# Kernel tuning notes

Measured on AMD Instinct MI355X. Metric: run time of the kernel, lower is better.

The kernel has to match this reference:

```python
import jax, jax.numpy as jnp
import numpy as np

N_NODES = 100000
N_EDGES = 1000000
IN_F, HID_F, OUT_F = 128, 128, 16


def setup_inputs() -> dict:
    key = jax.random.key(0)
    ks = jax.random.split(key, 8)
    x = jax.random.normal(ks[0], (N_NODES, IN_F), dtype=jnp.float32)
    src = jax.random.randint(ks[1], (N_EDGES,), 0, N_NODES, dtype=jnp.int64)
    dst = jax.random.randint(ks[2], (N_EDGES,), 0, N_NODES, dtype=jnp.int64)
    s = 1.0 / np.sqrt(HID_F)
    W1 = jax.random.normal(ks[3], (IN_F, HID_F), dtype=jnp.float32) * s
    W2 = jax.random.normal(ks[4], (HID_F, HID_F), dtype=jnp.float32) * s
    W3 = jax.random.normal(ks[5], (HID_F, HID_F), dtype=jnp.float32) * s
    W4 = jax.random.normal(ks[6], (HID_F, HID_F), dtype=jnp.float32) * s
    W5 = jax.random.normal(ks[7], (HID_F, OUT_F), dtype=jnp.float32) * s
    return {
        "x": x, "src": src, "dst": dst,
        "W1": W1, "b1": jnp.zeros((HID_F,), jnp.float32),
        "W2": W2, "b2": jnp.zeros((HID_F,), jnp.float32),
        "W3": W3, "b3": jnp.zeros((HID_F,), jnp.float32),
        "W4": W4, "b4": jnp.zeros((HID_F,), jnp.float32),
        "W5": W5, "b5": jnp.zeros((OUT_F,), jnp.float32),
    }


def reference(x, src, dst, W1, b1, W2, b2, W3, b3, W4, b4, W5, b5):
    N = x.shape[0]
    # in-degree per destination node (static graph, computed once)
    deg = jax.ops.segment_sum(jnp.ones_like(dst, dtype=x.dtype), dst, num_segments=N)
    inv = (1.0 / (deg + 1.0))[:, None]  # gcn aggregator normalizer: 1/(deg_in+1)

    def sage_gcn(h, W, b):
        # h_neigh[v] = (h[v] + sum_{u->v} h[u]) / (deg_in(v)+1); then linear
        agg = (h + jax.ops.segment_sum(h[src], dst, num_segments=N)) * inv
        return agg @ W + b

    h = jax.nn.relu(sage_gcn(x, W1, b1))
    h = jax.nn.relu(sage_gcn(h, W2, b2))
    h = jax.nn.relu(sage_gcn(h, W3, b3))
    h = jax.nn.relu(sage_gcn(h, W4, b4))
    h = sage_gcn(h, W5, b5)
    return jax.nn.log_softmax(h, axis=-1)
```

## Files before the change

### kernel.cpp

```cpp
#include <hip/hip_runtime.h>
#include <hip/hip_bf16.h>

#define NNODES 100000
#define NP (NNODES + 8)
#define NEDGES 1000000
#define HID 128
#define OUTF 16
#define NB 16
#define BCAP 81920
#define KB 64
#define BZT 1024
#define DB2 32
#define NBINS (NB * DB2)
#define NSL 4

typedef __attribute__((ext_vector_type(8))) short short8;
typedef __attribute__((ext_vector_type(4))) float floatx4;
typedef __attribute__((ext_vector_type(4))) unsigned int uintx4;
typedef unsigned int uint32;
typedef unsigned long long ull;
typedef unsigned short ushort16;

__device__ __forceinline__ float blo(uint32 u) { return __uint_as_float(u << 16); }
__device__ __forceinline__ float bhi(uint32 u) { return __uint_as_float(u & 0xffff0000u); }
__device__ __forceinline__ ushort16 f2b(float f) {
    __hip_bfloat16 h = __float2bfloat16(f);
    return *reinterpret_cast<ushort16*>(&h);
}
__device__ __forceinline__ uint32 pack2(float a, float b) {
    return (uint32)f2b(a) | ((uint32)f2b(b) << 16);
}


__global__ __launch_bounds__(BZT) void bucketize(const int* __restrict__ src,
                                                 const int* __restrict__ dst,
                                                 int* __restrict__ bcursor,
                                                 ull* __restrict__ stage, int E) {
    __shared__ int cnt[NB], lbase[NB], gbase[NB];
    __shared__ int2 buf[BZT];
    __shared__ unsigned char bb[BZT];
    int t = threadIdx.x;
    int e0 = blockIdx.x * BZT;
    int e = e0 + t;
    if (t < NB) cnt[t] = 0;
    __syncthreads();
    int s = 0, d = 0, b = 0, r = 0;
    bool valid = e < E;
    if (valid) {
        s = src[e];
        d = dst[e];
        b = (int)((unsigned)d * NB / NNODES);
        r = atomicAdd(&cnt[b], 1);
    }
    __syncthreads();
    if (t == 0) {
        int run = 0;
        for (int i = 0; i < NB; i++) { lbase[i] = run; run += cnt[i]; }
    }
    __syncthreads();
    if (valid) {
        int p = lbase[b] + r;
        buf[p] = make_int2(s, d);
        bb[p] = (unsigned char)b;
    }
    if (t < NB) gbase[t] = atomicAdd(&bcursor[t], cnt[t]);
    __syncthreads();
    int nvalid = min(BZT, E - e0);
    if (t < nvalid) {
        int b2 = bb[t];
        int2 sd = buf[t];
        int pos = gbase[b2] + (t - lbase[b2]);
        if (pos < BCAP) {
            ull val = (ull)(unsigned)sd.x | ((ull)(unsigned)sd.y << 32);
            __builtin_nontemporal_store(val, &stage[(size_t)b2 * BCAP + pos]);
        }
    }
}


__global__ __launch_bounds__(256) void count_rank(const ull* __restrict__ stage,
                                                  const int* __restrict__ bcursor,
                                                  int* __restrict__ counts,
                                                  int* __restrict__ rnk) {
    int blk = blockIdx.x;
    int b = (blk & 7) + 8 * ((blk >> 3) & 1);
    int slot = blk >> 4;
    int cntb = min(bcursor[b], BCAP);
    int per = (cntb + KB - 1) / KB;
    int s0 = slot * per;
    int s1 = min(s0 + per, cntb);
    const ull* st = stage + (size_t)b * BCAP;
    int* rk = rnk + (size_t)b * BCAP;
    for (int i = s0 + threadIdx.x; i < s1; i += 256) {
        ull v = st[i];
        int d = (int)(unsigned)(v >> 32);
        rk[i] = atomicAdd(&counts[d], 1);
    }
}


__global__ __launch_bounds__(256) void fill2(const ull* __restrict__ stage,
                                             const int* __restrict__ rnk,
                                             const int* __restrict__ bcursor,
                                             const int* __restrict__ perm,
                                             const int* __restrict__ offs,
                                             int* __restrict__ csr) {
    int blk = blockIdx.x;
    int b = (blk & 7) + 8 * ((blk >> 3) & 1);
    int slot = blk >> 4;
    int cntb = min(bcursor[b], BCAP);
    int per = (cntb + KB - 1) / KB;
    int s0 = slot * per;
    int s1 = min(s0 + per, cntb);
    const ull* st = stage + (size_t)b * BCAP;
    const int* rk = rnk + (size_t)b * BCAP;
    for (int i = s0 + threadIdx.x; i < s1; i += 256) {
        ull v = st[i];
        int s = (int)(v & 0xffffffffu);
        int d = (int)(unsigned)(v >> 32);
        int pd = perm[d];
        csr[offs[pd] + rk[i]] = perm[s];
    }
}


__global__ __launch_bounds__(256) void binhist(const int* __restrict__ counts,
                                               int* __restrict__ bins, int N) {
    __shared__ int h[NBINS];
    int t = threadIdx.x;
    for (int k = t; k < NBINS; k += 256) h[k] = 0;
    __syncthreads();
    int i = blockIdx.x * 256 + t;
    if (i < N) {
        int bi = (int)((unsigned)i * NB / NNODES);
        int db = min((counts[i] + 7) >> 3, DB2 - 1);
        atomicAdd(&h[bi * DB2 + db], 1);
    }
    __syncthreads();
    for (int k = t; k < NBINS; k += 256)
        if (h[k] > 0) atomicAdd(&bins[k], h[k]);
}

__global__ void binscan(int* __restrict__ bins) {
    if (threadIdx.x == 0) {
        int run = 0;
        for (int i = 0; i < NBINS; i++) {
            int c = bins[i];
            bins[i] = run;
            run += c;
        }
    }
}

__global__ __launch_bounds__(256) void dsort2(const int* __restrict__ counts,
                                              int* __restrict__ bins,
                                              int* __restrict__ perm,
                                              int* __restrict__ iperm,
                                              int* __restrict__ cnts_s, int N) {
    __shared__ int h[NBINS], lb[NBINS];
    int t = threadIdx.x;
    for (int k = t; k < NBINS; k += 256) h[k] = 0;
    __syncthreads();
    int i = blockIdx.x * 256 + t;
    int c = 0, idx = 0, r = 0;
    bool valid = i < N;
    if (valid) {
        c = counts[i];
        int bi = (int)((unsigned)i * NB / NNODES);
        idx = bi * DB2 + min((c + 7) >> 3, DB2 - 1);
        r = atomicAdd(&h[idx], 1);
    }
    __syncthreads();
    for (int k = t; k < NBINS; k += 256)
        lb[k] = (h[k] > 0) ? atomicAdd(&bins[k], h[k]) : 0;
    __syncthreads();
    if (valid) {
        int p = lb[idx] + r;
        perm[i] = p;
        iperm[p] = i;
        cnts_s[p] = c;
    }
}

__global__ void scan1(const int* __restrict__ cnts_s, int* __restrict__ offs,
                      int* __restrict__ bsum, int N) {
    __shared__ int tmp[256];
    int t = threadIdx.x;
    int i = blockIdx.x * 256 + t;
    int v = (i < N) ? ((cnts_s[i] + 7) & ~7) : 0;
    tmp[t] = v;
    __syncthreads();
    for (int d = 1; d < 256; d <<= 1) {
        int add = (t >= d) ? tmp[t - d] : 0;
        __syncthreads();
        tmp[t] += add;
        __syncthreads();
    }
    if (i < N) offs[i] = tmp[t] - v;
    if (t == 255) bsum[blockIdx.x] = tmp[255];
}

__global__ void scan2(int* __restrict__ bsum, int nb) {
    __shared__ int tmp[512];
    int t = threadIdx.x;
    int v = (t < nb) ? bsum[t] : 0;
    tmp[t] = v;
    __syncthreads();
    for (int d = 1; d < 512; d <<= 1) {
        int add = (t >= d) ? tmp[t - d] : 0;
        __syncthreads();
        tmp[t] += add;
        __syncthreads();
    }
    if (t < nb) bsum[t] = tmp[t] - v;
}

__global__ void scan3(int* __restrict__ offs, const int* __restrict__ bsum,
                      const int* __restrict__ cnts_s, float* __restrict__ invs,
                      int* __restrict__ csr, int N) {
    int i = blockIdx.x * 256 + threadIdx.x;
    if (i < N) {
        int o = offs[i] + bsum[blockIdx.x];
        offs[i] = o;
        int c = cnts_s[i];
        invs[i] = 1.0f / (float)(c + 1);
        int c8 = (c + 7) & ~7;
        for (int k = c; k < c8; k++) csr[o + k] = NNODES;
    }
}


__global__ void pack_all(const float* __restrict__ W1, const float* __restrict__ W2,
                         const float* __restrict__ W3, const float* __restrict__ W4,
                         ushort16* __restrict__ Wp1, ushort16* __restrict__ Wp2,
                         ushort16* __restrict__ Wp3, ushort16* __restrict__ Wp4,
                         uint32* __restrict__ zb, uint32* __restrict__ hb,
                         uint32* __restrict__ z16b) {
    int blk = blockIdx.x;
    int lane = threadIdx.x;
    if (blk < 128) {
        int w = blk >> 5, b = blk & 31;
        const float* W = w == 0 ? W1 : w == 1 ? W2 : w == 2 ? W3 : W4;
        ushort16* Wp = w == 0 ? Wp1 : w == 1 ? Wp2 : w == 2 ? Wp3 : Wp4;
        int nt = b >> 2, ks = b & 3;
        int n = nt * 16 + (lane & 15);
        int kbase = ks * 32 + ((lane >> 4) << 3);
        ushort16 tmp[8];
#pragma unroll
        for (int i = 0; i < 8; i++) tmp[i] = f2b(W[(size_t)(kbase + i) * HID + n]);
        *(uint4*)&Wp[((size_t)b * 64 + lane) * 8] = *(uint4*)tmp;
    } else {
        for (int i = lane; i < 4 * 8 * 16; i += 64) {
            int s = i >> 7, rem = i & 127, r = rem >> 4, k = rem & 15;
            zb[((size_t)s * NP + NNODES + r) * 16 + k] = 0;
            hb[((size_t)s * NP + NNODES + r) * 16 + k] = 0;
        }
        for (int i = lane; i < 64; i += 64)
            z16b[(size_t)(NNODES + (i >> 3)) * 8 + (i & 7)] = 0;
    }
}


template <int AF32>
__global__ __launch_bounds__(256) void gemm_mfma(const void* __restrict__ Av,
                                                 const int* __restrict__ iperm,
                                                 const ushort16* __restrict__ Wp,
                                                 ushort16* __restrict__ Z, int M) {
    __shared__ __align__(16) ushort16 Wl[32 * 64 * 8];
    int t = threadIdx.x;
    const uint4* wp4 = (const uint4*)Wp;
    uint4* wl4 = (uint4*)Wl;
#pragma unroll
    for (int p = 0; p < 8; p++) wl4[t + p * 256] = wp4[t + p * 256];
    __syncthreads();

    int wv = t >> 6, lane = t & 63;
    int row = blockIdx.x * 64 + wv * 16 + (lane & 15);
    int rowc = min(row, M - 1);
    int kb = (lane >> 4) << 3;

    short8 a[4];
    if (AF32) {
        const float* A = (const float*)Av;
        int orig = iperm[rowc];
#pragma unroll
        for (int ks = 0; ks < 4; ks++) {
            const float* p = A + (size_t)orig * HID + ks * 32 + kb;
            floatx4 lo = *(const floatx4*)p;
            floatx4 hi = *(const floatx4*)(p + 4);
            union { short8 s; ushort16 u[8]; } cv;
            cv.u[0] = f2b(lo.x); cv.u[1] = f2b(lo.y); cv.u[2] = f2b(lo.z); cv.u[3] = f2b(lo.w);
            cv.u[4] = f2b(hi.x); cv.u[5] = f2b(hi.y); cv.u[6] = f2b(hi.z); cv.u[7] = f2b(hi.w);
            a[ks] = cv.s;
        }
    } else {
        const ushort16* A = (const ushort16*)Av;
#pragma unroll
        for (int ks = 0; ks < 4; ks++)
            a[ks] = *(const short8*)(A + ((size_t)ks * NP + rowc) * 32 + kb);
    }

    floatx4 acc[8];
#pragma unroll
    for (int nt = 0; nt < 8; nt++) acc[nt] = (floatx4){0.f, 0.f, 0.f, 0.f};

#pragma unroll
    for (int nt = 0; nt < 8; nt++) {
#pragma unroll
        for (int ks = 0; ks < 4; ks++) {
            short8 w = *(const short8*)&Wl[(size_t)(((nt << 2) | ks) * 64 + lane) * 8];
            acc[nt] = __builtin_amdgcn_mfma_f32_16x16x32_bf16(w, a[ks], acc[nt], 0, 0, 0);
        }
    }

    if (row < M) {
        int c4 = (lane >> 4) << 2;
#pragma unroll
        for (int nt = 0; nt < 8; nt++) {
            int col = nt * 16 + c4;
            int sl = col >> 5, off = col & 31;
            union { ushort16 u[4]; uint2 v; } pk;
            pk.u[0] = f2b(acc[nt][0]);
            pk.u[1] = f2b(acc[nt][1]);
            pk.u[2] = f2b(acc[nt][2]);
            pk.u[3] = f2b(acc[nt][3]);
            *(uint2*)&Z[((size_t)sl * NP + row) * 32 + off] = pk.v;
        }
    }
}


#define ACCN(acc0, acc1, acc2, acc3, g)                \
    {                                                  \
        acc0.x += blo((g).x); acc0.y += bhi((g).x);    \
        acc1.x += blo((g).y); acc1.y += bhi((g).y);    \
        acc2.x += blo((g).z); acc2.y += bhi((g).z);    \
        acc3.x += blo((g).w); acc3.y += bhi((g).w);    \
    }

__global__ __launch_bounds__(256) void agg_sliced(const uint32* __restrict__ Z,
                                                  const int* __restrict__ offs,
                                                  const int* __restrict__ cnts_s,
                                                  const int* __restrict__ csr,
                                                  const float* __restrict__ invs,
                                                  const float* __restrict__ bias,
                                                  uint32* __restrict__ H, int N) {
    int s = blockIdx.x & 3;
    int chunk = blockIdx.x >> 2;
    int t = threadIdx.x;
    int l = t & 3;
    int p = chunk * 64 + (t >> 2);
    bool act = p < N;
    int pc = act ? p : N - 1;
    const uint4* Zs = (const uint4*)(Z + (size_t)s * NP * 16);
    uint4* Hs = (uint4*)(H + (size_t)s * NP * 16);

    int beg = offs[pc];
    int cnt8 = (cnts_s[pc] + 7) & ~7;
    float sc = invs[pc];

    uint4 sv = Zs[(size_t)pc * 4 + l];
    float2 acc0 = make_float2(blo(sv.x), bhi(sv.x));
    float2 acc1 = make_float2(blo(sv.y), bhi(sv.y));
    float2 acc2 = make_float2(blo(sv.z), bhi(sv.z));
    float2 acc3 = make_float2(blo(sv.w), bhi(sv.w));

    for (int j = 0; j < cnt8; j += 8) {
        int4 ia = *(const int4*)&csr[beg + j];
        int4 ib = *(const int4*)&csr[beg + j + 4];
        uint4 g[8];
        g[0] = Zs[(size_t)ia.x * 4 + l];
        g[1] = Zs[(size_t)ia.y * 4 + l];
        g[2] = Zs[(size_t)ia.z * 4 + l];
        g[3] = Zs[(size_t)ia.w * 4 + l];
        g[4] = Zs[(size_t)ib.x * 4 + l];
        g[5] = Zs[(size_t)ib.y * 4 + l];
        g[6] = Zs[(size_t)ib.z * 4 + l];
        g[7] = Zs[(size_t)ib.w * 4 + l];
#pragma unroll
        for (int q = 0; q < 8; q++) ACCN(acc0, acc1, acc2, acc3, g[q]);
    }

    const float* bp = bias + s * 32 + l * 8;
    floatx4 b01 = *(const floatx4*)bp;
    floatx4 b23 = *(const floatx4*)(bp + 4);
    uintx4 o;
    o.x = pack2(fmaxf(acc0.x * sc + b01.x, 0.f), fmaxf(acc0.y * sc + b01.y, 0.f));
    o.y = pack2(fmaxf(acc1.x * sc + b01.z, 0.f), fmaxf(acc1.y * sc + b01.w, 0.f));
    o.z = pack2(fmaxf(acc2.x * sc + b23.x, 0.f), fmaxf(acc2.y * sc + b23.y, 0.f));
    o.w = pack2(fmaxf(acc3.x * sc + b23.z, 0.f), fmaxf(acc3.y * sc + b23.w, 0.f));
    if (act) __builtin_nontemporal_store(o, (uintx4*)&Hs[(size_t)p * 4 + l]);
}


__global__ __launch_bounds__(256) void gemm16(const uint32* __restrict__ A,
                                              const float* __restrict__ W5,
                                              uint32* __restrict__ Z16, int M) {
    __shared__ float Ws[HID * OUTF];
    int t = threadIdx.x;
    for (int i = t; i < HID * OUTF; i += 256) Ws[i] = W5[i];
    __syncthreads();
    int gid = blockIdx.x * 256 + t;
    int r = gid >> 3, cp = gid & 7;
    if (r >= M) return;
    float a0 = 0.f, a1 = 0.f;
#pragma unroll
    for (int s4 = 0; s4 < 4; s4++) {
        const uint32* ar = A + ((size_t)s4 * NP + r) * 16;
#pragma unroll
        for (int k = 0; k < 16; k++) {
            uint32 u = ar[k];
            float f0 = blo(u), f1 = bhi(u);
            a0 += f0 * Ws[(s4 * 32 + 2 * k) * OUTF + 2 * cp] +
                  f1 * Ws[(s4 * 32 + 2 * k + 1) * OUTF + 2 * cp];
            a1 += f0 * Ws[(s4 * 32 + 2 * k) * OUTF + 2 * cp + 1] +
                  f1 * Ws[(s4 * 32 + 2 * k + 1) * OUTF + 2 * cp + 1];
        }
    }
    Z16[(size_t)r * 8 + cp] = pack2(a0, a1);
}


__global__ __launch_bounds__(256) void agg16_lsm(const uint32* __restrict__ Z16,
                                                 const int* __restrict__ offs,
                                                 const int* __restrict__ cnts_s,
                                                 const int* __restrict__ csr,
                                                 const float* __restrict__ invs,
                                                 const int* __restrict__ iperm,
                                                 const float* __restrict__ b5,
                                                 float* __restrict__ out, int N) {
    int t = threadIdx.x;
    int l = t & 1;
    int p = blockIdx.x * 128 + (t >> 1);
    bool act = p < N;
    int pc = act ? p : N - 1;
    const uint4* Zs = (const uint4*)Z16;

    uint4 sv = Zs[(size_t)pc * 2 + l];
    float2 acc0 = make_float2(blo(sv.x), bhi(sv.x));
    float2 acc1 = make_float2(blo(sv.y), bhi(sv.y));
    float2 acc2 = make_float2(blo(sv.z), bhi(sv.z));
    float2 acc3 = make_float2(blo(sv.w), bhi(sv.w));

    int beg = offs[pc];
    int cnt8 = (cnts_s[pc] + 7) & ~7;
    for (int j = 0; j < cnt8; j += 8) {
        int4 ia = *(const int4*)&csr[beg + j];
        int4 ib = *(const int4*)&csr[beg + j + 4];
        uint4 g[8];
        g[0] = Zs[(size_t)ia.x * 2 + l];
        g[1] = Zs[(size_t)ia.y * 2 + l];
        g[2] = Zs[(size_t)ia.z * 2 + l];
        g[3] = Zs[(size_t)ia.w * 2 + l];
        g[4] = Zs[(size_t)ib.x * 2 + l];
        g[5] = Zs[(size_t)ib.y * 2 + l];
        g[6] = Zs[(size_t)ib.z * 2 + l];
        g[7] = Zs[(size_t)ib.w * 2 + l];
#pragma unroll
        for (int q = 0; q < 8; q++) ACCN(acc0, acc1, acc2, acc3, g[q]);
    }

    float sc = invs[pc];
    const float* bp = b5 + l * 8;
    floatx4 b01 = *(const floatx4*)bp;
    floatx4 b23 = *(const floatx4*)(bp + 4);
    float val[8];
    val[0] = acc0.x * sc + b01.x; val[1] = acc0.y * sc + b01.y;
    val[2] = acc1.x * sc + b01.z; val[3] = acc1.y * sc + b01.w;
    val[4] = acc2.x * sc + b23.x; val[5] = acc2.y * sc + b23.y;
    val[6] = acc3.x * sc + b23.z; val[7] = acc3.y * sc + b23.w;
    float mm = val[0];
#pragma unroll
    for (int k = 1; k < 8; k++) mm = fmaxf(mm, val[k]);
    mm = fmaxf(mm, __shfl_xor(mm, 1, 64));
    float ss = 0.f;
#pragma unroll
    for (int k = 0; k < 8; k++) ss += expf(val[k] - mm);
    ss += __shfl_xor(ss, 1, 64);
    float ls = mm + logf(ss);
    if (act) {
        int ov = iperm[p];
        float4 o0 = make_float4(val[0] - ls, val[1] - ls, val[2] - ls, val[3] - ls);
        float4 o1 = make_float4(val[4] - ls, val[5] - ls, val[6] - ls, val[7] - ls);
        float* op = out + (size_t)ov * OUTF + l * 8;
        *(float4*)op = o0;
        *(float4*)(op + 4) = o1;
    }
}


extern "C" void kernel_launch(void* const* d_in, const int* in_sizes, int n_in,
                              void* d_out, int out_size, void* d_ws, size_t ws_size,
                              hipStream_t stream) {
    const float* x   = (const float*)d_in[0];
    const int*   src = (const int*)d_in[1];
    const int*   dst = (const int*)d_in[2];
    const float* W1 = (const float*)d_in[3];
    const float* b1 = (const float*)d_in[4];
    const float* W2 = (const float*)d_in[5];
    const float* b2 = (const float*)d_in[6];
    const float* W3 = (const float*)d_in[7];
    const float* b3 = (const float*)d_in[8];
    const float* W4 = (const float*)d_in[9];
    const float* b4 = (const float*)d_in[10];
    const float* W5 = (const float*)d_in[11];
    const float* b5 = (const float*)d_in[12];

    char* ws = (char*)d_ws;
    size_t off = 0;
    auto alloc = [&](size_t bytes) {
        void* p = ws + off;
        off = (off + bytes + 255) & ~(size_t)255;
        return p;
    };
    const size_t CSR_ELEMS = (size_t)NEDGES + 7 * (size_t)NNODES + 64;
    ushort16* zb   = (ushort16*)alloc((size_t)NSL * NP * 32 * 2);
    ushort16* hb   = (ushort16*)alloc((size_t)NSL * NP * 32 * 2);
    uint32*   z16b = (uint32*)alloc((size_t)NP * OUTF * 2);
    int*      counts = (int*)alloc((size_t)NNODES * 4);
    int*      cnts_s = (int*)alloc((size_t)NNODES * 4);
    int*      perm   = (int*)alloc((size_t)NNODES * 4);
    int*      iperm  = (int*)alloc((size_t)NNODES * 4);
    float*    invs   = (float*)alloc((size_t)NNODES * 4);
    int*      offs   = (int*)alloc((size_t)(NNODES + 1) * 4);
    int*      bsum   = (int*)alloc(512 * 4);
    int*      csr    = (int*)alloc(CSR_ELEMS * 4);
    ull*      stage  = (ull*)alloc((size_t)NB * BCAP * 8);
    int*      rnk    = (int*)alloc((size_t)NB * BCAP * 4);
    int*      bcursor = (int*)alloc((NB + NBINS) * 4);
    int*      bins   = bcursor + NB;
    ushort16* Wp1 = (ushort16*)alloc((size_t)HID * HID * 2);
    ushort16* Wp2 = (ushort16*)alloc((size_t)HID * HID * 2);
    ushort16* Wp3 = (ushort16*)alloc((size_t)HID * HID * 2);
    ushort16* Wp4 = (ushort16*)alloc((size_t)HID * HID * 2);
    (void)ws_size; (void)in_sizes; (void)n_in; (void)out_size;

    const int N = NNODES, E = NEDGES;
    int nb = (N + 255) / 256;

    hipMemsetAsync(counts, 0, (size_t)N * 4, stream);
    hipMemsetAsync(bcursor, 0, (NB + NBINS) * 4, stream);
    bucketize<<<(E + BZT - 1) / BZT, BZT, 0, stream>>>(src, dst, bcursor, stage, E);
    count_rank<<<NB * KB, 256, 0, stream>>>(stage, bcursor, counts, rnk);
    binhist<<<nb, 256, 0, stream>>>(counts, bins, N);
    binscan<<<1, 64, 0, stream>>>(bins);
    dsort2<<<nb, 256, 0, stream>>>(counts, bins, perm, iperm, cnts_s, N);
    scan1<<<nb, 256, 0, stream>>>(cnts_s, offs, bsum, N);
    scan2<<<1, 512, 0, stream>>>(bsum, nb);
    scan3<<<nb, 256, 0, stream>>>(offs, bsum, cnts_s, invs, csr, N);
    fill2<<<NB * KB, 256, 0, stream>>>(stage, rnk, bcursor, perm, offs, csr);
    pack_all<<<129, 64, 0, stream>>>(W1, W2, W3, W4, Wp1, Wp2, Wp3, Wp4,
                                     (uint32*)zb, (uint32*)hb, z16b);

    int gemmGrid = (N + 63) / 64;
    int aggGrid  = NSL * ((N + 63) / 64);
    int agg16Grid = (N + 127) / 128;

    gemm_mfma<1><<<gemmGrid, 256, 0, stream>>>((const void*)x, iperm, Wp1, zb, N);
    agg_sliced<<<aggGrid, 256, 0, stream>>>((const uint32*)zb, offs, cnts_s, csr, invs, b1,
                                            (uint32*)hb, N);

    gemm_mfma<0><<<gemmGrid, 256, 0, stream>>>((const void*)hb, nullptr, Wp2, zb, N);
    agg_sliced<<<aggGrid, 256, 0, stream>>>((const uint32*)zb, offs, cnts_s, csr, invs, b2,
                                            (uint32*)hb, N);

    gemm_mfma<0><<<gemmGrid, 256, 0, stream>>>((const void*)hb, nullptr, Wp3, zb, N);
    agg_sliced<<<aggGrid, 256, 0, stream>>>((const uint32*)zb, offs, cnts_s, csr, invs, b3,
                                            (uint32*)hb, N);

    gemm_mfma<0><<<gemmGrid, 256, 0, stream>>>((const void*)hb, nullptr, Wp4, zb, N);
    agg_sliced<<<aggGrid, 256, 0, stream>>>((const uint32*)zb, offs, cnts_s, csr, invs, b4,
                                            (uint32*)hb, N);

    gemm16<<<(N * 8 + 255) / 256, 256, 0, stream>>>((const uint32*)hb, W5, z16b, N);
    agg16_lsm<<<agg16Grid, 256, 0, stream>>>(z16b, offs, cnts_s, csr, invs, iperm, b5,
                                             (float*)d_out, N);
}
```

Measured before the change: 371.6 us.

## Build CSR with per-bucket shared-memory histograms and process 256 rows per GEMM block

```diff
diff --git a/kernel.cpp b/kernel.cpp
--- a/kernel.cpp
+++ b/kernel.cpp
@@ -7,8 +7,8 @@
 #define HID 128
 #define OUTF 16
 #define NB 16
+#define NBKT (NNODES / NB)
 #define BCAP 81920
-#define KB 64
 #define BZT 1024
 #define DB2 32
 #define NBINS (NB * DB2)
@@ -49,7 +49,7 @@
     if (valid) {
         s = src[e];
         d = dst[e];
-        b = (int)((unsigned)d * NB / NNODES);
+        b = d / NBKT;
         r = atomicAdd(&cnt[b], 1);
     }
     __syncthreads();
@@ -78,48 +78,43 @@
 }
 
 
-__global__ __launch_bounds__(256) void count_rank(const ull* __restrict__ stage,
-                                                  const int* __restrict__ bcursor,
-                                                  int* __restrict__ counts,
-                                                  int* __restrict__ rnk) {
-    int blk = blockIdx.x;
-    int b = (blk & 7) + 8 * ((blk >> 3) & 1);
-    int slot = blk >> 4;
+__global__ __launch_bounds__(1024) void bhist(const ull* __restrict__ stage,
+                                              const int* __restrict__ bcursor,
+                                              int* __restrict__ counts) {
+    __shared__ int h[NBKT];
+    int b = blockIdx.x;
+    int base = b * NBKT;
+    for (int i = threadIdx.x; i < NBKT; i += 1024) h[i] = 0;
+    __syncthreads();
     int cntb = min(bcursor[b], BCAP);
-    int per = (cntb + KB - 1) / KB;
-    int s0 = slot * per;
-    int s1 = min(s0 + per, cntb);
     const ull* st = stage + (size_t)b * BCAP;
-    int* rk = rnk + (size_t)b * BCAP;
-    for (int i = s0 + threadIdx.x; i < s1; i += 256) {
-        ull v = st[i];
-        int d = (int)(unsigned)(v >> 32);
-        rk[i] = atomicAdd(&counts[d], 1);
-    }
-}
-
-
-__global__ __launch_bounds__(256) void fill2(const ull* __restrict__ stage,
-                                             const int* __restrict__ rnk,
-                                             const int* __restrict__ bcursor,
-                                             const int* __restrict__ perm,
-                                             const int* __restrict__ offs,
-                                             int* __restrict__ csr) {
-    int blk = blockIdx.x;
-    int b = (blk & 7) + 8 * ((blk >> 3) & 1);
-    int slot = blk >> 4;
+    for (int i = threadIdx.x; i < cntb; i += 1024) {
+        int d = (int)(unsigned)(st[i] >> 32);
+        atomicAdd(&h[d - base], 1);
+    }
+    __syncthreads();
+    for (int i = threadIdx.x; i < NBKT; i += 1024) counts[base + i] = h[i];
+}
+
+
+__global__ __launch_bounds__(1024) void bfill(const ull* __restrict__ stage,
+                                              const int* __restrict__ bcursor,
+                                              const int* __restrict__ perm,
+                                              const int* __restrict__ offs,
+                                              int* __restrict__ csr) {
+    __shared__ int cur[NBKT];
+    int b = blockIdx.x;
+    int base = b * NBKT;
+    for (int i = threadIdx.x; i < NBKT; i += 1024) cur[i] = 0;
+    __syncthreads();
     int cntb = min(bcursor[b], BCAP);
-    int per = (cntb + KB - 1) / KB;
-    int s0 = slot * per;
-    int s1 = min(s0 + per, cntb);
     const ull* st = stage + (size_t)b * BCAP;
-    const int* rk = rnk + (size_t)b * BCAP;
-    for (int i = s0 + threadIdx.x; i < s1; i += 256) {
+    for (int i = threadIdx.x; i < cntb; i += 1024) {
         ull v = st[i];
         int s = (int)(v & 0xffffffffu);
         int d = (int)(unsigned)(v >> 32);
-        int pd = perm[d];
-        csr[offs[pd] + rk[i]] = perm[s];
+        int r = atomicAdd(&cur[d - base], 1);
+        csr[offs[perm[d]] + r] = perm[s];
     }
 }
 
@@ -132,7 +127,7 @@
     __syncthreads();
     int i = blockIdx.x * 256 + t;
     if (i < N) {
-        int bi = (int)((unsigned)i * NB / NNODES);
+        int bi = i / NBKT;
         int db = min((counts[i] + 7) >> 3, DB2 - 1);
         atomicAdd(&h[bi * DB2 + db], 1);
     }
@@ -166,7 +161,7 @@
     bool valid = i < N;
     if (valid) {
         c = counts[i];
-        int bi = (int)((unsigned)i * NB / NNODES);
+        int bi = i / NBKT;
         idx = bi * DB2 + min((c + 7) >> 3, DB2 - 1);
         r = atomicAdd(&h[idx], 1);
     }
@@ -275,56 +270,59 @@
     __syncthreads();
 
     int wv = t >> 6, lane = t & 63;
-    int row = blockIdx.x * 64 + wv * 16 + (lane & 15);
-    int rowc = min(row, M - 1);
     int kb = (lane >> 4) << 3;
-
-    short8 a[4];
-    if (AF32) {
-        const float* A = (const float*)Av;
-        int orig = iperm[rowc];
-#pragma unroll
-        for (int ks = 0; ks < 4; ks++) {
-            const float* p = A + (size_t)orig * HID + ks * 32 + kb;
-            floatx4 lo = *(const floatx4*)p;
-            floatx4 hi = *(const floatx4*)(p + 4);
-            union { short8 s; ushort16 u[8]; } cv;
-            cv.u[0] = f2b(lo.x); cv.u[1] = f2b(lo.y); cv.u[2] = f2b(lo.z); cv.u[3] = f2b(lo.w);
-            cv.u[4] = f2b(hi.x); cv.u[5] = f2b(hi.y); cv.u[6] = f2b(hi.z); cv.u[7] = f2b(hi.w);
-            a[ks] = cv.s;
-        }
-    } else {
-        const ushort16* A = (const ushort16*)Av;
-#pragma unroll
-        for (int ks = 0; ks < 4; ks++)
-            a[ks] = *(const short8*)(A + ((size_t)ks * NP + rowc) * 32 + kb);
-    }
-
-    floatx4 acc[8];
-#pragma unroll
-    for (int nt = 0; nt < 8; nt++) acc[nt] = (floatx4){0.f, 0.f, 0.f, 0.f};
-
-#pragma unroll
-    for (int nt = 0; nt < 8; nt++) {
-#pragma unroll
-        for (int ks = 0; ks < 4; ks++) {
-            short8 w = *(const short8*)&Wl[(size_t)(((nt << 2) | ks) * 64 + lane) * 8];
-            acc[nt] = __builtin_amdgcn_mfma_f32_16x16x32_bf16(w, a[ks], acc[nt], 0, 0, 0);
-        }
-    }
-
-    if (row < M) {
-        int c4 = (lane >> 4) << 2;
+    int c4 = (lane >> 4) << 2;
+
+    for (int rt = 0; rt < 4; rt++) {
+        int row = blockIdx.x * 256 + rt * 64 + wv * 16 + (lane & 15);
+        int rowc = min(row, M - 1);
+
+        short8 a[4];
+        if (AF32) {
+            const float* A = (const float*)Av;
+            int orig = iperm[rowc];
+#pragma unroll
+            for (int ks = 0; ks < 4; ks++) {
+                const float* p = A + (size_t)orig * HID + ks * 32 + kb;
+                floatx4 lo = *(const floatx4*)p;
+                floatx4 hi = *(const floatx4*)(p + 4);
+                union { short8 s; ushort16 u[8]; } cv;
+                cv.u[0] = f2b(lo.x); cv.u[1] = f2b(lo.y); cv.u[2] = f2b(lo.z); cv.u[3] = f2b(lo.w);
+                cv.u[4] = f2b(hi.x); cv.u[5] = f2b(hi.y); cv.u[6] = f2b(hi.z); cv.u[7] = f2b(hi.w);
+                a[ks] = cv.s;
+            }
+        } else {
+            const ushort16* A = (const ushort16*)Av;
+#pragma unroll
+            for (int ks = 0; ks < 4; ks++)
+                a[ks] = *(const short8*)(A + ((size_t)ks * NP + rowc) * 32 + kb);
+        }
+
+        floatx4 acc[8];
+#pragma unroll
+        for (int nt = 0; nt < 8; nt++) acc[nt] = (floatx4){0.f, 0.f, 0.f, 0.f};
+
 #pragma unroll
         for (int nt = 0; nt < 8; nt++) {
-            int col = nt * 16 + c4;
-            int sl = col >> 5, off = col & 31;
-            union { ushort16 u[4]; uint2 v; } pk;
-            pk.u[0] = f2b(acc[nt][0]);
-            pk.u[1] = f2b(acc[nt][1]);
-            pk.u[2] = f2b(acc[nt][2]);
-            pk.u[3] = f2b(acc[nt][3]);
-            *(uint2*)&Z[((size_t)sl * NP + row) * 32 + off] = pk.v;
+#pragma unroll
+            for (int ks = 0; ks < 4; ks++) {
+                short8 w = *(const short8*)&Wl[(size_t)(((nt << 2) | ks) * 64 + lane) * 8];
+                acc[nt] = __builtin_amdgcn_mfma_f32_16x16x32_bf16(w, a[ks], acc[nt], 0, 0, 0);
+            }
+        }
+
+        if (row < M) {
+#pragma unroll
+            for (int nt = 0; nt < 8; nt++) {
+                int col = nt * 16 + c4;
+                int sl = col >> 5, off = col & 31;
+                union { ushort16 u[4]; uint2 v; } pk;
+                pk.u[0] = f2b(acc[nt][0]);
+                pk.u[1] = f2b(acc[nt][1]);
+                pk.u[2] = f2b(acc[nt][2]);
+                pk.u[3] = f2b(acc[nt][3]);
+                *(uint2*)&Z[((size_t)sl * NP + row) * 32 + off] = pk.v;
+            }
         }
     }
 }
@@ -526,7 +524,6 @@
     int*      bsum   = (int*)alloc(512 * 4);
     int*      csr    = (int*)alloc(CSR_ELEMS * 4);
     ull*      stage  = (ull*)alloc((size_t)NB * BCAP * 8);
-    int*      rnk    = (int*)alloc((size_t)NB * BCAP * 4);
     int*      bcursor = (int*)alloc((NB + NBINS) * 4);
     int*      bins   = bcursor + NB;
     ushort16* Wp1 = (ushort16*)alloc((size_t)HID * HID * 2);
@@ -538,21 +535,20 @@
     const int N = NNODES, E = NEDGES;
     int nb = (N + 255) / 256;
 
-    hipMemsetAsync(counts, 0, (size_t)N * 4, stream);
     hipMemsetAsync(bcursor, 0, (NB + NBINS) * 4, stream);
     bucketize<<<(E + BZT - 1) / BZT, BZT, 0, stream>>>(src, dst, bcursor, stage, E);
-    count_rank<<<NB * KB, 256, 0, stream>>>(stage, bcursor, counts, rnk);
+    bhist<<<NB, 1024, 0, stream>>>(stage, bcursor, counts);
     binhist<<<nb, 256, 0, stream>>>(counts, bins, N);
     binscan<<<1, 64, 0, stream>>>(bins);
     dsort2<<<nb, 256, 0, stream>>>(counts, bins, perm, iperm, cnts_s, N);
     scan1<<<nb, 256, 0, stream>>>(cnts_s, offs, bsum, N);
     scan2<<<1, 512, 0, stream>>>(bsum, nb);
     scan3<<<nb, 256, 0, stream>>>(offs, bsum, cnts_s, invs, csr, N);
-    fill2<<<NB * KB, 256, 0, stream>>>(stage, rnk, bcursor, perm, offs, csr);
+    bfill<<<NB, 1024, 0, stream>>>(stage, bcursor, perm, offs, csr);
     pack_all<<<129, 64, 0, stream>>>(W1, W2, W3, W4, Wp1, Wp2, Wp3, Wp4,
                                      (uint32*)zb, (uint32*)hb, z16b);
 
-    int gemmGrid = (N + 63) / 64;
+    int gemmGrid = (N + 255) / 256;
     int aggGrid  = NSL * ((N + 63) / 64);
     int agg16Grid = (N + 127) / 128;
 
```

After: 482.2 us. 1.3x slower.
